# Performance work log

Hardware: AMD Instinct MI355X
Metric: run time of the kernel (lower is better)

The kernel has to match this reference:

```python
import jax, jax.numpy as jnp
import numpy as np

N, E = 50000, 800000
D_NODE, D_EDGE, D_EF = 128, 64, 16
IN_CH = D_NODE + D_EDGE + D_EF  # 208, lin2 input
EPS = 1e-5


def setup_inputs() -> dict:
    key = jax.random.key(0)
    ks = jax.random.split(key, 20)
    s = lambda k, shp: jax.random.normal(k, shp, jnp.float32) * 0.05
    return {
        "x": jax.random.normal(ks[0], (N, D_NODE), jnp.float32),
        "edge_index": jax.random.randint(ks[1], (2, E), 0, N, jnp.int32),
        "edge_f": jax.random.normal(ks[2], (E, D_EF), jnp.float32),
        "edge_attr": jax.random.normal(ks[3], (E, D_EDGE), jnp.float32),
        "lin1_w": s(ks[4], (D_NODE, D_NODE)), "lin1_b": jnp.zeros((D_NODE,), jnp.float32),
        "lin2_w": s(ks[5], (IN_CH, D_EDGE)), "lin2_b": jnp.zeros((D_EDGE,), jnp.float32),
        "linw_w": s(ks[6], (D_EDGE, 1)), "linw_b": jnp.zeros((1,), jnp.float32),
        "gcn_w": s(ks[7], (D_NODE, D_NODE)), "gcn_b": jnp.zeros((D_NODE,), jnp.float32),
        "bn_e_g": jnp.ones((D_EDGE,), jnp.float32), "bn_e_b": jnp.zeros((D_EDGE,), jnp.float32),
        "bn_n_g": jnp.ones((D_NODE,), jnp.float32), "bn_n_b": jnp.zeros((D_NODE,), jnp.float32),
    }


def reference(x, edge_index, edge_f, edge_attr,
              lin1_w, lin1_b, lin2_w, lin2_b, linw_w, linw_b,
              gcn_w, gcn_b, bn_e_g, bn_e_b, bn_n_g, bn_n_b):
    src, dst = edge_index[0], edge_index[1]  # x_j = x[src], x_i = x[dst]
    n_nodes = x.shape[0]

    # Edgeconvf: vectorized gather + shared lin1 on both endpoints
    h = x @ lin1_w + lin1_b                       # [N, D_NODE]
    x_em = jax.nn.relu(h[src] + h[dst])           # [E, D_NODE]
    feat = jnp.concatenate([x_em, edge_attr, edge_f], axis=-1)  # [E, 208]
    ef = feat @ lin2_w + lin2_b                   # [E, D_EDGE]

    # BatchNorm1d over edges (training-mode batch stats, biased var)
    mu = ef.mean(axis=0)
    var = ef.var(axis=0)
    ef = (ef - mu) * jax.lax.rsqrt(var + EPS) * bn_e_g + bn_e_b
    ef = jax.nn.relu(ef)

    # edge weights
    w = jax.nn.relu(ef @ linw_w + linw_b)[:, 0]   # [E]

    # GCNConv with edge_weight, self-loops (fill weight 1), sym norm
    xw = x @ gcn_w                                # [N, D_NODE]
    deg = jax.ops.segment_sum(w, dst, num_segments=n_nodes) + 1.0
    dinv = jnp.where(deg > 0, jax.lax.rsqrt(deg), 0.0)
    norm = dinv[src] * w * dinv[dst]              # [E]
    agg = jax.ops.segment_sum(norm[:, None] * xw[src], dst, num_segments=n_nodes)
    x1 = agg + (dinv * dinv)[:, None] * xw + gcn_b  # self loop norm = dinv_i^2

    # BatchNorm over nodes, relu, residuals
    mu_n = x1.mean(axis=0)
    var_n = x1.var(axis=0)
    x1 = (x1 - mu_n) * jax.lax.rsqrt(var_n + EPS) * bn_n_g + bn_n_b
    x1 = jax.nn.relu(x1)

    return (x1 + x, ef + edge_attr)
```

## Files before the change

### kernel.cpp

```cpp
#include <hip/hip_runtime.h>


#define NN 50000
#define NE 800000
#define DN 128
#define DE 64
#define DF 16
#define KP 232
#define KP1 136
#define EPS 1e-5f
#define SCAN_BLOCKS 49

typedef float f32x4 __attribute__((ext_vector_type(4)));
typedef short s16x8 __attribute__((ext_vector_type(8)));
typedef unsigned short u16;

__device__ __forceinline__ float bf2f(u16 u) {
  union { unsigned int i; float f; } v; v.i = ((unsigned int)u) << 16; return v.f;
}
__device__ __forceinline__ u16 f2bf(float f) {
  union { float ff; unsigned int i; } v; v.ff = f;
  unsigned int x = v.i;
  return (u16)((x + 0x7fffu + ((x >> 16) & 1u)) >> 16);
}

__global__ void kpre_x(const float* __restrict__ x, u16* __restrict__ xbf) {
  int tot = NN * DN / 4;
  for (int i = blockIdx.x * blockDim.x + threadIdx.x; i < tot; i += gridDim.x * blockDim.x) {
    float4 v = ((const float4*)x)[i];
    ushort4 o;
    o.x = f2bf(v.x); o.y = f2bf(v.y); o.z = f2bf(v.z); o.w = f2bf(v.w);
    ((ushort4*)xbf)[i] = o;
  }
}

__global__ void kpre_w(const float* __restrict__ lin1w, const float* __restrict__ gcnw,
                       const float* __restrict__ lin2w,
                       u16* __restrict__ WcatT, u16* __restrict__ l2wT) {
  int t = threadIdx.x;
  for (int k = 0; k < DN; ++k) {
    float v = (t < DN) ? lin1w[k * DN + t] : gcnw[k * DN + (t - DN)];
    WcatT[t * DN + k] = f2bf(v);
  }
  if (t < DE) {
    for (int k = 0; k < KP; ++k) {
      float v = (k < (DN + DE + DF)) ? lin2w[k * DE + t] : 0.f;
      l2wT[t * KP + k] = f2bf(v);
    }
  }
}

__global__ void khist(const int* __restrict__ ei, int* __restrict__ cnt) {
  for (int i = blockIdx.x * blockDim.x + threadIdx.x; i < NE; i += gridDim.x * blockDim.x)
    atomicAdd(&cnt[ei[NE + i]], 1);
}

__global__ void kscan1(const int* __restrict__ cnt, int* __restrict__ rowst, int* __restrict__ blks) {
  __shared__ int ls[256];
  int b = blockIdx.x, t = threadIdx.x;
  int base = b * 1024 + t * 4;
  int c0 = base     < NN ? cnt[base]     : 0;
  int c1 = base + 1 < NN ? cnt[base + 1] : 0;
  int c2 = base + 2 < NN ? cnt[base + 2] : 0;
  int c3 = base + 3 < NN ? cnt[base + 3] : 0;
  int s = c0 + c1 + c2 + c3;
  ls[t] = s; __syncthreads();
  for (int off = 1; off < 256; off <<= 1) {
    int v = (t >= off) ? ls[t - off] : 0;
    __syncthreads();
    ls[t] += v;
    __syncthreads();
  }
  int excl = ls[t] - s;
  if (t == 255) blks[b] = ls[255];
  if (base     < NN) rowst[base]     = excl;
  if (base + 1 < NN) rowst[base + 1] = excl + c0;
  if (base + 2 < NN) rowst[base + 2] = excl + c0 + c1;
  if (base + 3 < NN) rowst[base + 3] = excl + c0 + c1 + c2;
}

__global__ void kscan2(int* __restrict__ blks) {
  if (threadIdx.x == 0) {
    int run = 0;
    for (int i = 0; i < SCAN_BLOCKS; ++i) { int v = blks[i]; blks[i] = run; run += v; }
  }
}

__global__ void kscan3(const int* __restrict__ blks, int* __restrict__ rowst, int* __restrict__ cur) {
  int b = blockIdx.x, t = threadIdx.x;
  int add = blks[b];
  int base = b * 1024 + t * 4;
#pragma unroll
  for (int j = 0; j < 4; ++j) {
    int i = base + j;
    if (i < NN) { int v = rowst[i] + add; rowst[i] = v; cur[i] = v; }
  }
  if (b == 0 && t == 0) rowst[NN] = NE;
}

__global__ void kscat(const int* __restrict__ ei, int* __restrict__ cur, int* __restrict__ csr) {
  for (int i = blockIdx.x * blockDim.x + threadIdx.x; i < NE; i += gridDim.x * blockDim.x) {
    int n = ei[NE + i];
    int p = atomicAdd(&cur[n], 1);
    csr[p] = i;
  }
}

__global__ void __launch_bounds__(256) k_nodegemm(
    const u16* __restrict__ xbf, const u16* __restrict__ WcatT,
    const float* __restrict__ lin1b,
    u16* __restrict__ hbf, float* __restrict__ xw)
{
  __shared__ __align__(16) u16 As[64 * KP1];
  __shared__ __align__(16) u16 Bs[64 * KP1];
  int tid = threadIdx.x;
  int tile = blockIdx.x >> 2, ct = blockIdx.x & 3;
  int n0 = tile * 64, c0 = ct * 64;
  int r = tid >> 2, q = tid & 3;
  {
    int n = n0 + r;
    s16x8* dst = (s16x8*)(As + r * KP1 + q * 32);
    if (n < NN) {
      const s16x8* src = (const s16x8*)(xbf + n * DN + q * 32);
      dst[0] = src[0]; dst[1] = src[1]; dst[2] = src[2]; dst[3] = src[3];
    } else {
      s16x8 z = {0,0,0,0,0,0,0,0};
      dst[0] = z; dst[1] = z; dst[2] = z; dst[3] = z;
    }
    const s16x8* bsrc = (const s16x8*)(WcatT + (c0 + r) * DN + q * 32);
    s16x8* bdst = (s16x8*)(Bs + r * KP1 + q * 32);
    bdst[0] = bsrc[0]; bdst[1] = bsrc[1]; bdst[2] = bsrc[2]; bdst[3] = bsrc[3];
  }
  __syncthreads();
  int w = tid >> 6, l = tid & 63, lr = l & 15, lg = l >> 4;
  f32x4 acc[4] = {{0,0,0,0},{0,0,0,0},{0,0,0,0},{0,0,0,0}};
  for (int kt = 0; kt < 4; ++kt) {
    s16x8 av = *(const s16x8*)(As + (w * 16 + lr) * KP1 + kt * 32 + lg * 8);
#pragma unroll
    for (int nt = 0; nt < 4; ++nt) {
      s16x8 bv = *(const s16x8*)(Bs + (nt * 16 + lr) * KP1 + kt * 32 + lg * 8);
      acc[nt] = __builtin_amdgcn_mfma_f32_16x16x32_bf16(av, bv, acc[nt], 0, 0, 0);
    }
  }
#pragma unroll
  for (int nt = 0; nt < 4; ++nt) {
    int gcol = c0 + nt * 16 + lr;
#pragma unroll
    for (int rr = 0; rr < 4; ++rr) {
      int n = n0 + w * 16 + lg * 4 + rr;
      if (n < NN) {
        float v = acc[nt][rr];
        if (gcol < DN) hbf[n * DN + gcol] = f2bf(v + lin1b[gcol]);
        else           xw[n * DN + (gcol - DN)] = v;
      }
    }
  }
}

__global__ void __launch_bounds__(256) k_lin2(
    const int* __restrict__ ei, const float* __restrict__ eattr,
    const float* __restrict__ efeat, const u16* __restrict__ hbf,
    const u16* __restrict__ l2wT, const float* __restrict__ lin2b,
    float* __restrict__ efraw)
{
  __shared__ __align__(16) u16 As[64 * KP];
  __shared__ __align__(16) u16 Bs[64 * KP];
  int tid = threadIdx.x;
  int e0 = blockIdx.x * 64;
  {
    const float4* bs = (const float4*)l2wT;
    float4* bd = (float4*)Bs;
    for (int i = tid; i < 64 * KP * 2 / 16; i += 256) bd[i] = bs[i];
  }
  {
    int el = tid >> 2, t = tid & 3;
    int e = e0 + el;
    int sn = ei[e], dn = ei[NE + e];
    const s16x8* hs = (const s16x8*)(hbf + sn * DN + t * 32);
    const s16x8* hd = (const s16x8*)(hbf + dn * DN + t * 32);
    s16x8* dst = (s16x8*)(As + el * KP + t * 32);
#pragma unroll
    for (int j = 0; j < 4; ++j) {
      s16x8 a = hs[j], b = hd[j];
      s16x8 o;
#pragma unroll
      for (int i = 0; i < 8; ++i) {
        float v = bf2f((u16)a[i]) + bf2f((u16)b[i]);
        o[i] = (short)f2bf(fmaxf(v, 0.f));
      }
      dst[j] = o;
    }
    if (t < 2) {
      const float4* ap = (const float4*)(eattr + (long)e * DE + t * 32);
      s16x8* ad = (s16x8*)(As + el * KP + DN + t * 32);
#pragma unroll
      for (int j = 0; j < 4; ++j) {
        float4 v0 = ap[2 * j], v1 = ap[2 * j + 1];
        s16x8 o;
        o[0] = (short)f2bf(v0.x); o[1] = (short)f2bf(v0.y);
        o[2] = (short)f2bf(v0.z); o[3] = (short)f2bf(v0.w);
        o[4] = (short)f2bf(v1.x); o[5] = (short)f2bf(v1.y);
        o[6] = (short)f2bf(v1.z); o[7] = (short)f2bf(v1.w);
        ad[j] = o;
      }
    } else if (t == 2) {
      const float4* fp = (const float4*)(efeat + (long)e * DF);
      s16x8* fd = (s16x8*)(As + el * KP + DN + DE);
#pragma unroll
      for (int j = 0; j < 2; ++j) {
        float4 v0 = fp[2 * j], v1 = fp[2 * j + 1];
        s16x8 o;
        o[0] = (short)f2bf(v0.x); o[1] = (short)f2bf(v0.y);
        o[2] = (short)f2bf(v0.z); o[3] = (short)f2bf(v0.w);
        o[4] = (short)f2bf(v1.x); o[5] = (short)f2bf(v1.y);
        o[6] = (short)f2bf(v1.z); o[7] = (short)f2bf(v1.w);
        fd[j] = o;
      }
    } else {
      s16x8 z = {0,0,0,0,0,0,0,0};
      s16x8* zd = (s16x8*)(As + el * KP + 208);
      zd[0] = z; zd[1] = z; zd[2] = z;
    }
  }
  __syncthreads();
  int w = tid >> 6, l = tid & 63, lr = l & 15, lg = l >> 4;
  f32x4 acc[4] = {{0,0,0,0},{0,0,0,0},{0,0,0,0},{0,0,0,0}};
  for (int kt = 0; kt < 7; ++kt) {
    s16x8 av = *(const s16x8*)(As + (w * 16 + lr) * KP + kt * 32 + lg * 8);
#pragma unroll
    for (int nt = 0; nt < 4; ++nt) {
      s16x8 bv = *(const s16x8*)(Bs + (nt * 16 + lr) * KP + kt * 32 + lg * 8);
      acc[nt] = __builtin_amdgcn_mfma_f32_16x16x32_bf16(av, bv, acc[nt], 0, 0, 0);
    }
  }
#pragma unroll
  for (int nt = 0; nt < 4; ++nt) {
    int col = nt * 16 + lr;
    float bb = lin2b[col];
#pragma unroll
    for (int rr = 0; rr < 4; ++rr) {
      int e = e0 + w * 16 + lg * 4 + rr;
      efraw[(long)e * DE + col] = acc[nt][rr] + bb;
    }
  }
}

__global__ void k_estat(const float* __restrict__ efraw, float* __restrict__ est) {
  int tid = threadIdx.x;
  int c = tid & 63, sub = tid >> 6;
  float s = 0.f, q = 0.f;
  for (long e = blockIdx.x * 4 + sub; e < NE; e += (long)gridDim.x * 4) {
    float v = efraw[e * DE + c];
    s += v; q += v * v;
  }
  __shared__ float lsS[256], lsQ[256];
  lsS[tid] = s; lsQ[tid] = q;
  __syncthreads();
  if (tid < 64) {
    s = lsS[tid] + lsS[tid + 64] + lsS[tid + 128] + lsS[tid + 192];
    q = lsQ[tid] + lsQ[tid + 64] + lsQ[tid + 128] + lsQ[tid + 192];
    int rep = (blockIdx.x & 7) * 128;
    atomicAdd(&est[rep + c], s);
    atomicAdd(&est[rep + 64 + c], q);
  }
}

__global__ void k_estat_fin(const float* __restrict__ est, const float* __restrict__ g,
                            const float* __restrict__ b, float* __restrict__ eab) {
  int c = threadIdx.x;
  if (c < DE) {
    float s = 0.f, q = 0.f;
    for (int r = 0; r < 8; ++r) { s += est[r * 128 + c]; q += est[r * 128 + 64 + c]; }
    float mu = s / (float)NE;
    float var = q / (float)NE - mu * mu;
    float a = rsqrtf(var + EPS) * g[c];
    eab[c] = a;
    eab[DE + c] = b[c] - mu * a;
  }
}

__global__ void k_edge2(const float* __restrict__ eattr, const float* __restrict__ eab,
                        const float* __restrict__ linw, const float* __restrict__ linwb,
                        float* __restrict__ efio, float* __restrict__ wbuf)
{
  long e = blockIdx.x * 4 + (threadIdx.x >> 6);
  int c = threadIdx.x & 63;
  float v = efio[e * DE + c];
  float efn = fmaxf(v * eab[c] + eab[DE + c], 0.f);
  efio[e * DE + c] = efn + eattr[e * DE + c];
  float p = efn * linw[c];
#pragma unroll
  for (int off = 32; off > 0; off >>= 1) p += __shfl_xor(p, off);
  if (c == 0) wbuf[e] = fmaxf(p + linwb[0], 0.f);
}

__global__ void k_deg(const int* __restrict__ rowst, const int* __restrict__ csr,
                      const float* __restrict__ wbuf, float* __restrict__ dinv)
{
  int n = blockIdx.x * 4 + (threadIdx.x >> 6);
  int lane = threadIdx.x & 63;
  int a = rowst[n], b = rowst[n + 1];
  float s = 0.f;
  for (int i = a + lane; i < b; i += 64) s += wbuf[csr[i]];
#pragma unroll
  for (int off = 32; off > 0; off >>= 1) s += __shfl_xor(s, off);
  if (lane == 0) dinv[n] = rsqrtf(s + 1.0f);
}

__global__ void __launch_bounds__(128) k_agg(
    const int* __restrict__ ei, const int* __restrict__ rowst, const int* __restrict__ csr,
    const float* __restrict__ wbuf, const float* __restrict__ dinv,
    const float* __restrict__ xw, const float* __restrict__ gcnb,
    float* __restrict__ x1)
{
  int n = blockIdx.x, c = threadIdx.x;
  int a = rowst[n], b = rowst[n + 1];
  float acc = 0.f;
  for (int i = a; i < b; ++i) {
    int eid = csr[i];
    int s = ei[eid];
    acc += wbuf[eid] * dinv[s] * xw[s * DN + c];
  }
  float di = dinv[n];
  x1[n * DN + c] = acc * di + di * di * xw[n * DN + c] + gcnb[c];
}

__global__ void k_nstat(const float* __restrict__ x1, float* __restrict__ nst) {
  int tid = threadIdx.x;
  int c = tid & 127, sub = tid >> 7;
  float s = 0.f, q = 0.f;
  for (int n = blockIdx.x * 2 + sub; n < NN; n += gridDim.x * 2) {
    float v = x1[n * DN + c];
    s += v; q += v * v;
  }
  __shared__ float lsS[256], lsQ[256];
  lsS[tid] = s; lsQ[tid] = q;
  __syncthreads();
  if (tid < 128) {
    s = lsS[tid] + lsS[tid + 128];
    q = lsQ[tid] + lsQ[tid + 128];
    int rep = (blockIdx.x & 7) * 256;
    atomicAdd(&nst[rep + c], s);
    atomicAdd(&nst[rep + 128 + c], q);
  }
}

__global__ void k_nstat_fin(const float* __restrict__ nst, const float* __restrict__ g,
                            const float* __restrict__ b, float* __restrict__ nab) {
  int c = threadIdx.x;
  if (c < DN) {
    float s = 0.f, q = 0.f;
    for (int r = 0; r < 8; ++r) { s += nst[r * 256 + c]; q += nst[r * 256 + 128 + c]; }
    float mu = s / (float)NN;
    float var = q / (float)NN - mu * mu;
    float a = rsqrtf(var + EPS) * g[c];
    nab[c] = a;
    nab[DN + c] = b[c] - mu * a;
  }
}

__global__ void k_out0(const float* __restrict__ x1, const float* __restrict__ x,
                       const float* __restrict__ nab, float* __restrict__ out0)
{
  int i = blockIdx.x * 256 + threadIdx.x;
  int c0 = (i * 4) & 127;
  float4 v = ((const float4*)x1)[i];
  float4 xv = ((const float4*)x)[i];
  float4 av = *(const float4*)(nab + c0);
  float4 bv = *(const float4*)(nab + DN + c0);
  float4 o;
  o.x = fmaxf(v.x * av.x + bv.x, 0.f) + xv.x;
  o.y = fmaxf(v.y * av.y + bv.y, 0.f) + xv.y;
  o.z = fmaxf(v.z * av.z + bv.z, 0.f) + xv.z;
  o.w = fmaxf(v.w * av.w + bv.w, 0.f) + xv.w;
  ((float4*)out0)[i] = o;
}

extern "C" void kernel_launch(void* const* d_in, const int* in_sizes, int n_in,
                              void* d_out, int out_size, void* d_ws, size_t ws_size,
                              hipStream_t stream)
{
  const float* x     = (const float*)d_in[0];
  const int*   ei    = (const int*)d_in[1];
  const float* efeat = (const float*)d_in[2];
  const float* eattr = (const float*)d_in[3];
  const float* lin1w = (const float*)d_in[4];
  const float* lin1b = (const float*)d_in[5];
  const float* lin2w = (const float*)d_in[6];
  const float* lin2b = (const float*)d_in[7];
  const float* linw  = (const float*)d_in[8];
  const float* linwb = (const float*)d_in[9];
  const float* gcnw  = (const float*)d_in[10];
  const float* gcnb  = (const float*)d_in[11];
  const float* beg   = (const float*)d_in[12];
  const float* beb   = (const float*)d_in[13];
  const float* bng   = (const float*)d_in[14];
  const float* bnb   = (const float*)d_in[15];

  char* wsp = (char*)d_ws;
  size_t off = 0;
  auto alloc = [&](size_t b) { char* p = wsp + off; off += (b + 255) & ~(size_t)255; return p; };
  u16*   xbf    = (u16*)  alloc((size_t)NN * DN * 2);
  u16*   hbf    = (u16*)  alloc((size_t)NN * DN * 2);
  float* xw     = (float*)alloc((size_t)NN * DN * 4);
  float* x1     = (float*)alloc((size_t)NN * DN * 4);
  float* wbuf   = (float*)alloc((size_t)NE * 4);
  int*   csr    = (int*)  alloc((size_t)NE * 4);
  int*   rowst  = (int*)  alloc((size_t)(NN + 1) * 4);
  int*   cur    = (int*)  alloc((size_t)NN * 4);
  float* dinv   = (float*)alloc((size_t)NN * 4);
  int*   blks   = (int*)  alloc(64 * 4);
  u16*   WcatT  = (u16*)  alloc(256 * 128 * 2);
  u16*   l2wT   = (u16*)  alloc(64 * KP * 2);
  float* est    = (float*)alloc(8 * 128 * 4);
  float* eab    = (float*)alloc(128 * 4);
  float* nst    = (float*)alloc(8 * 256 * 4);
  float* nab    = (float*)alloc(256 * 4);

  float* out0  = (float*)d_out;
  float* efraw = (float*)d_out + (size_t)NN * DN;

  hipMemsetAsync(cur, 0, (size_t)NN * 4, stream);
  hipMemsetAsync(est, 0, 8 * 128 * 4, stream);
  hipMemsetAsync(nst, 0, 8 * 256 * 4, stream);

  kpre_x<<<1024, 256, 0, stream>>>(x, xbf);
  kpre_w<<<1, 256, 0, stream>>>(lin1w, gcnw, lin2w, WcatT, l2wT);
  khist<<<1024, 256, 0, stream>>>(ei, cur);
  kscan1<<<SCAN_BLOCKS, 256, 0, stream>>>(cur, rowst, blks);
  kscan2<<<1, 64, 0, stream>>>(blks);
  kscan3<<<SCAN_BLOCKS, 256, 0, stream>>>(blks, rowst, cur);
  kscat<<<1024, 256, 0, stream>>>(ei, cur, csr);
  k_nodegemm<<<782 * 4, 256, 0, stream>>>(xbf, WcatT, lin1b, hbf, xw);
  k_lin2<<<NE / 64, 256, 0, stream>>>(ei, eattr, efeat, hbf, l2wT, lin2b, efraw);
  k_estat<<<1024, 256, 0, stream>>>(efraw, est);
  k_estat_fin<<<1, 64, 0, stream>>>(est, beg, beb, eab);
  k_edge2<<<NE / 4, 256, 0, stream>>>(eattr, eab, linw, linwb, efraw, wbuf);
  k_deg<<<NN / 4, 256, 0, stream>>>(rowst, csr, wbuf, dinv);
  k_agg<<<NN, 128, 0, stream>>>(ei, rowst, csr, wbuf, dinv, xw, gcnb, x1);
  k_nstat<<<1024, 256, 0, stream>>>(x1, nst);
  k_nstat_fin<<<1, 128, 0, stream>>>(nst, bng, bnb, nab);
  k_out0<<<NN * DN / 1024, 256, 0, stream>>>(x1, x, nab, out0);
}
```

Baseline: 1.188 ms.

## Fuse edge BN stats into lin2, fold x conversion, precompute CSR coefficients

Several changes land together. The x-to-bf16 conversion moves into the node GEMM load, and the lin2 weights are pre-swizzled into MFMA fragment order so they are read straight from global/L2 instead of being staged in shared memory. Edge batch-norm statistics are reduced inside the lin2 epilogue, with 16 atomic replicas, which removes a full re-read of the edge features. Degree is now accumulated with float atomics in k_edge2 rather than a CSR pass, and per-CSR source/coefficient arrays are precomputed so aggregation does fewer dependent gathers. The costs are contended atomics on degree and nondeterministic float summation order.

```diff
diff --git a/kernel.cpp b/kernel.cpp
--- a/kernel.cpp
+++ b/kernel.cpp
@@ -7,9 +7,11 @@
 #define DE 64
 #define DF 16
 #define KP 232
+#define NKT 7
 #define KP1 136
 #define EPS 1e-5f
 #define SCAN_BLOCKS 49
+#define EREP 16
 
 typedef float f32x4 __attribute__((ext_vector_type(4)));
 typedef short s16x8 __attribute__((ext_vector_type(8)));
@@ -24,29 +26,26 @@
   return (u16)((x + 0x7fffu + ((x >> 16) & 1u)) >> 16);
 }
 
-__global__ void kpre_x(const float* __restrict__ x, u16* __restrict__ xbf) {
-  int tot = NN * DN / 4;
-  for (int i = blockIdx.x * blockDim.x + threadIdx.x; i < tot; i += gridDim.x * blockDim.x) {
-    float4 v = ((const float4*)x)[i];
-    ushort4 o;
-    o.x = f2bf(v.x); o.y = f2bf(v.y); o.z = f2bf(v.z); o.w = f2bf(v.w);
-    ((ushort4*)xbf)[i] = o;
-  }
-}
-
 __global__ void kpre_w(const float* __restrict__ lin1w, const float* __restrict__ gcnw,
                        const float* __restrict__ lin2w,
-                       u16* __restrict__ WcatT, u16* __restrict__ l2wT) {
+                       u16* __restrict__ WcatT, u16* __restrict__ l2wF) {
   int t = threadIdx.x;
   for (int k = 0; k < DN; ++k) {
     float v = (t < DN) ? lin1w[k * DN + t] : gcnw[k * DN + (t - DN)];
     WcatT[t * DN + k] = f2bf(v);
   }
-  if (t < DE) {
-    for (int k = 0; k < KP; ++k) {
-      float v = (k < (DN + DE + DF)) ? lin2w[k * DE + t] : 0.f;
-      l2wT[t * KP + k] = f2bf(v);
-    }
+  for (int f = t; f < NKT * 256; f += 256) {
+    int kt = f >> 8, s = f & 255;
+    int nt = s >> 6, l = s & 63;
+    int lg = l >> 4, lr = l & 15;
+    int col = nt * 16 + lr;
+    s16x8 o;
+#pragma unroll
+    for (int j = 0; j < 8; ++j) {
+      int k = kt * 32 + lg * 8 + j;
+      o[j] = (short)((k < (DN + DE + DF)) ? f2bf(lin2w[k * DE + col]) : (u16)0);
+    }
+    ((s16x8*)l2wF)[f] = o;
   }
 }
 
@@ -107,7 +106,7 @@
 }
 
 __global__ void __launch_bounds__(256) k_nodegemm(
-    const u16* __restrict__ xbf, const u16* __restrict__ WcatT,
+    const float* __restrict__ x, const u16* __restrict__ WcatT,
     const float* __restrict__ lin1b,
     u16* __restrict__ hbf, float* __restrict__ xw)
 {
@@ -121,8 +120,17 @@
     int n = n0 + r;
     s16x8* dst = (s16x8*)(As + r * KP1 + q * 32);
     if (n < NN) {
-      const s16x8* src = (const s16x8*)(xbf + n * DN + q * 32);
-      dst[0] = src[0]; dst[1] = src[1]; dst[2] = src[2]; dst[3] = src[3];
+      const float4* src = (const float4*)(x + (long)n * DN + q * 32);
+#pragma unroll
+      for (int j = 0; j < 4; ++j) {
+        float4 v0 = src[2 * j], v1 = src[2 * j + 1];
+        s16x8 o;
+        o[0] = (short)f2bf(v0.x); o[1] = (short)f2bf(v0.y);
+        o[2] = (short)f2bf(v0.z); o[3] = (short)f2bf(v0.w);
+        o[4] = (short)f2bf(v1.x); o[5] = (short)f2bf(v1.y);
+        o[6] = (short)f2bf(v1.z); o[7] = (short)f2bf(v1.w);
+        dst[j] = o;
+      }
     } else {
       s16x8 z = {0,0,0,0,0,0,0,0};
       dst[0] = z; dst[1] = z; dst[2] = z; dst[3] = z;
@@ -160,18 +168,14 @@
 __global__ void __launch_bounds__(256) k_lin2(
     const int* __restrict__ ei, const float* __restrict__ eattr,
     const float* __restrict__ efeat, const u16* __restrict__ hbf,
-    const u16* __restrict__ l2wT, const float* __restrict__ lin2b,
-    float* __restrict__ efraw)
+    const u16* __restrict__ l2wF, const float* __restrict__ lin2b,
+    float* __restrict__ efraw, float* __restrict__ est)
 {
   __shared__ __align__(16) u16 As[64 * KP];
-  __shared__ __align__(16) u16 Bs[64 * KP];
+  __shared__ float sS[4][4][16];
+  __shared__ float sQ[4][4][16];
   int tid = threadIdx.x;
   int e0 = blockIdx.x * 64;
-  {
-    const float4* bs = (const float4*)l2wT;
-    float4* bd = (float4*)Bs;
-    for (int i = tid; i < 64 * KP * 2 / 16; i += 256) bd[i] = bs[i];
-  }
   {
     int el = tid >> 2, t = tid & 3;
     int e = e0 + el;
@@ -225,11 +229,12 @@
   __syncthreads();
   int w = tid >> 6, l = tid & 63, lr = l & 15, lg = l >> 4;
   f32x4 acc[4] = {{0,0,0,0},{0,0,0,0},{0,0,0,0},{0,0,0,0}};
-  for (int kt = 0; kt < 7; ++kt) {
+#pragma unroll
+  for (int kt = 0; kt < NKT; ++kt) {
     s16x8 av = *(const s16x8*)(As + (w * 16 + lr) * KP + kt * 32 + lg * 8);
 #pragma unroll
     for (int nt = 0; nt < 4; ++nt) {
-      s16x8 bv = *(const s16x8*)(Bs + (nt * 16 + lr) * KP + kt * 32 + lg * 8);
+      s16x8 bv = ((const s16x8*)l2wF)[(kt * 4 + nt) * 64 + l];
       acc[nt] = __builtin_amdgcn_mfma_f32_16x16x32_bf16(av, bv, acc[nt], 0, 0, 0);
     }
   }
@@ -237,31 +242,26 @@
   for (int nt = 0; nt < 4; ++nt) {
     int col = nt * 16 + lr;
     float bb = lin2b[col];
+    float sv = 0.f, qv = 0.f;
 #pragma unroll
     for (int rr = 0; rr < 4; ++rr) {
       int e = e0 + w * 16 + lg * 4 + rr;
-      efraw[(long)e * DE + col] = acc[nt][rr] + bb;
-    }
-  }
-}
-
-__global__ void k_estat(const float* __restrict__ efraw, float* __restrict__ est) {
-  int tid = threadIdx.x;
-  int c = tid & 63, sub = tid >> 6;
-  float s = 0.f, q = 0.f;
-  for (long e = blockIdx.x * 4 + sub; e < NE; e += (long)gridDim.x * 4) {
-    float v = efraw[e * DE + c];
-    s += v; q += v * v;
-  }
-  __shared__ float lsS[256], lsQ[256];
-  lsS[tid] = s; lsQ[tid] = q;
+      float v = acc[nt][rr] + bb;
+      efraw[(long)e * DE + col] = v;
+      sv += v; qv += v * v;
+    }
+    sv += __shfl_xor(sv, 16); sv += __shfl_xor(sv, 32);
+    qv += __shfl_xor(qv, 16); qv += __shfl_xor(qv, 32);
+    if (lg == 0) { sS[w][nt][lr] = sv; sQ[w][nt][lr] = qv; }
+  }
   __syncthreads();
-  if (tid < 64) {
-    s = lsS[tid] + lsS[tid + 64] + lsS[tid + 128] + lsS[tid + 192];
-    q = lsQ[tid] + lsQ[tid + 64] + lsQ[tid + 128] + lsQ[tid + 192];
-    int rep = (blockIdx.x & 7) * 128;
-    atomicAdd(&est[rep + c], s);
-    atomicAdd(&est[rep + 64 + c], q);
+  if (tid < DE) {
+    int nt = tid >> 4, lr2 = tid & 15;
+    float s = sS[0][nt][lr2] + sS[1][nt][lr2] + sS[2][nt][lr2] + sS[3][nt][lr2];
+    float q = sQ[0][nt][lr2] + sQ[1][nt][lr2] + sQ[2][nt][lr2] + sQ[3][nt][lr2];
+    int rep = (blockIdx.x & (EREP - 1)) * 128;
+    atomicAdd(&est[rep + tid], s);
+    atomicAdd(&est[rep + 64 + tid], q);
   }
 }
 
@@ -270,7 +270,7 @@
   int c = threadIdx.x;
   if (c < DE) {
     float s = 0.f, q = 0.f;
-    for (int r = 0; r < 8; ++r) { s += est[r * 128 + c]; q += est[r * 128 + 64 + c]; }
+    for (int r = 0; r < EREP; ++r) { s += est[r * 128 + c]; q += est[r * 128 + 64 + c]; }
     float mu = s / (float)NE;
     float var = q / (float)NE - mu * mu;
     float a = rsqrtf(var + EPS) * g[c];
@@ -279,9 +279,11 @@
   }
 }
 
-__global__ void k_edge2(const float* __restrict__ eattr, const float* __restrict__ eab,
+__global__ void k_edge2(const int* __restrict__ ei,
+                        const float* __restrict__ eattr, const float* __restrict__ eab,
                         const float* __restrict__ linw, const float* __restrict__ linwb,
-                        float* __restrict__ efio, float* __restrict__ wbuf)
+                        float* __restrict__ efio, float* __restrict__ wbuf,
+                        float* __restrict__ deg)
 {
   long e = blockIdx.x * 4 + (threadIdx.x >> 6);
   int c = threadIdx.x & 63;
@@ -291,25 +293,34 @@
   float p = efn * linw[c];
 #pragma unroll
   for (int off = 32; off > 0; off >>= 1) p += __shfl_xor(p, off);
-  if (c == 0) wbuf[e] = fmaxf(p + linwb[0], 0.f);
-}
-
-__global__ void k_deg(const int* __restrict__ rowst, const int* __restrict__ csr,
-                      const float* __restrict__ wbuf, float* __restrict__ dinv)
-{
-  int n = blockIdx.x * 4 + (threadIdx.x >> 6);
-  int lane = threadIdx.x & 63;
-  int a = rowst[n], b = rowst[n + 1];
-  float s = 0.f;
-  for (int i = a + lane; i < b; i += 64) s += wbuf[csr[i]];
-#pragma unroll
-  for (int off = 32; off > 0; off >>= 1) s += __shfl_xor(s, off);
-  if (lane == 0) dinv[n] = rsqrtf(s + 1.0f);
+  if (c == 0) {
+    float wv = fmaxf(p + linwb[0], 0.f);
+    wbuf[e] = wv;
+    atomicAdd(&deg[ei[NE + e]], wv);
+  }
+}
+
+__global__ void k_dinv(const float* __restrict__ deg, float* __restrict__ dinv) {
+  int i = blockIdx.x * 256 + threadIdx.x;
+  if (i < NN) dinv[i] = rsqrtf(deg[i] + 1.0f);
+}
+
+__global__ void k_coef(const int* __restrict__ csr, const int* __restrict__ ei,
+                       const float* __restrict__ wbuf, const float* __restrict__ dinv,
+                       int* __restrict__ csrsrc, float* __restrict__ csrcoef)
+{
+  int i = blockIdx.x * 256 + threadIdx.x;
+  if (i < NE) {
+    int eid = csr[i];
+    int s = ei[eid];
+    csrsrc[i] = s;
+    csrcoef[i] = wbuf[eid] * dinv[s];
+  }
 }
 
 __global__ void __launch_bounds__(128) k_agg(
-    const int* __restrict__ ei, const int* __restrict__ rowst, const int* __restrict__ csr,
-    const float* __restrict__ wbuf, const float* __restrict__ dinv,
+    const int* __restrict__ rowst, const int* __restrict__ csrsrc,
+    const float* __restrict__ csrcoef, const float* __restrict__ dinv,
     const float* __restrict__ xw, const float* __restrict__ gcnb,
     float* __restrict__ x1)
 {
@@ -317,9 +328,7 @@
   int a = rowst[n], b = rowst[n + 1];
   float acc = 0.f;
   for (int i = a; i < b; ++i) {
-    int eid = csr[i];
-    int s = ei[eid];
-    acc += wbuf[eid] * dinv[s] * xw[s * DN + c];
+    acc += csrcoef[i] * xw[(long)csrsrc[i] * DN + c];
   }
   float di = dinv[n];
   x1[n * DN + c] = acc * di + di * di * xw[n * DN + c] + gcnb[c];
@@ -400,19 +409,21 @@
   char* wsp = (char*)d_ws;
   size_t off = 0;
   auto alloc = [&](size_t b) { char* p = wsp + off; off += (b + 255) & ~(size_t)255; return p; };
-  u16*   xbf    = (u16*)  alloc((size_t)NN * DN * 2);
   u16*   hbf    = (u16*)  alloc((size_t)NN * DN * 2);
   float* xw     = (float*)alloc((size_t)NN * DN * 4);
   float* x1     = (float*)alloc((size_t)NN * DN * 4);
   float* wbuf   = (float*)alloc((size_t)NE * 4);
   int*   csr    = (int*)  alloc((size_t)NE * 4);
+  int*   csrsrc = (int*)  alloc((size_t)NE * 4);
+  float* csrcoef= (float*)alloc((size_t)NE * 4);
   int*   rowst  = (int*)  alloc((size_t)(NN + 1) * 4);
   int*   cur    = (int*)  alloc((size_t)NN * 4);
   float* dinv   = (float*)alloc((size_t)NN * 4);
+  float* deg    = (float*)alloc((size_t)NN * 4);
   int*   blks   = (int*)  alloc(64 * 4);
   u16*   WcatT  = (u16*)  alloc(256 * 128 * 2);
-  u16*   l2wT   = (u16*)  alloc(64 * KP * 2);
-  float* est    = (float*)alloc(8 * 128 * 4);
+  u16*   l2wF   = (u16*)  alloc((size_t)NKT * 256 * 8 * 2);
+  float* est    = (float*)alloc(EREP * 128 * 4);
   float* eab    = (float*)alloc(128 * 4);
   float* nst    = (float*)alloc(8 * 256 * 4);
   float* nab    = (float*)alloc(256 * 4);
@@ -421,23 +432,23 @@
   float* efraw = (float*)d_out + (size_t)NN * DN;
 
   hipMemsetAsync(cur, 0, (size_t)NN * 4, stream);
-  hipMemsetAsync(est, 0, 8 * 128 * 4, stream);
+  hipMemsetAsync(deg, 0, (size_t)NN * 4, stream);
+  hipMemsetAsync(est, 0, EREP * 128 * 4, stream);
   hipMemsetAsync(nst, 0, 8 * 256 * 4, stream);
 
-  kpre_x<<<1024, 256, 0, stream>>>(x, xbf);
-  kpre_w<<<1, 256, 0, stream>>>(lin1w, gcnw, lin2w, WcatT, l2wT);
+  kpre_w<<<1, 256, 0, stream>>>(lin1w, gcnw, lin2w, WcatT, l2wF);
   khist<<<1024, 256, 0, stream>>>(ei, cur);
   kscan1<<<SCAN_BLOCKS, 256, 0, stream>>>(cur, rowst, blks);
   kscan2<<<1, 64, 0, stream>>>(blks);
   kscan3<<<SCAN_BLOCKS, 256, 0, stream>>>(blks, rowst, cur);
   kscat<<<1024, 256, 0, stream>>>(ei, cur, csr);
-  k_nodegemm<<<782 * 4, 256, 0, stream>>>(xbf, WcatT, lin1b, hbf, xw);
-  k_lin2<<<NE / 64, 256, 0, stream>>>(ei, eattr, efeat, hbf, l2wT, lin2b, efraw);
-  k_estat<<<1024, 256, 0, stream>>>(efraw, est);
+  k_nodegemm<<<782 * 4, 256, 0, stream>>>(x, WcatT, lin1b, hbf, xw);
+  k_lin2<<<NE / 64, 256, 0, stream>>>(ei, eattr, efeat, hbf, l2wF, lin2b, efraw, est);
   k_estat_fin<<<1, 64, 0, stream>>>(est, beg, beb, eab);
-  k_edge2<<<NE / 4, 256, 0, stream>>>(eattr, eab, linw, linwb, efraw, wbuf);
-  k_deg<<<NN / 4, 256, 0, stream>>>(rowst, csr, wbuf, dinv);
-  k_agg<<<NN, 128, 0, stream>>>(ei, rowst, csr, wbuf, dinv, xw, gcnb, x1);
+  k_edge2<<<NE / 4, 256, 0, stream>>>(ei, eattr, eab, linw, linwb, efraw, wbuf, deg);
+  k_dinv<<<(NN + 255) / 256, 256, 0, stream>>>(deg, dinv);
+  k_coef<<<(NE + 255) / 256, 256, 0, stream>>>(csr, ei, wbuf, dinv, csrsrc, csrcoef);
+  k_agg<<<NN, 128, 0, stream>>>(rowst, csrsrc, csrcoef, dinv, xw, gcnb, x1);
   k_nstat<<<1024, 256, 0, stream>>>(x1, nst);
   k_nstat_fin<<<1, 128, 0, stream>>>(nst, bng, bnb, nab);
   k_out0<<<NN * DN / 1024, 256, 0, stream>>>(x1, x, nab, out0);
```

Result: faster. 1.024 ms (-13.8%).
